# Optimization experiments

Hardware: AMD Instinct MI355X
Metric: run time of the kernel (lower is better)

The kernel has to match this reference:

```python
import jax, jax.numpy as jnp
import numpy as np

HEADS = 8
DIM_HEAD = 64
EPS = 1e-4
SCALE = DIM_HEAD ** -0.5


def setup_inputs() -> dict:
    key = jax.random.key(0)
    k1, k2, k3, k4 = jax.random.split(key, 4)
    dim = HEADS * DIM_HEAD  # 512
    x = jax.random.normal(k1, (2, 2048, dim), dtype=jnp.float32)
    # torch Linear weights are [out, in]; scale like default init
    Wq = jax.random.normal(k2, (dim, dim), dtype=jnp.float32) / np.sqrt(dim)
    Wkv = jax.random.normal(k3, (2 * dim, dim), dtype=jnp.float32) / np.sqrt(dim)
    Wout = jax.random.normal(k4, (dim, dim), dtype=jnp.float32) / np.sqrt(dim)
    return {"x": x, "Wq": Wq, "Wkv": Wkv, "Wout": Wout}


def _normalize_magnitude(t, eps=EPS):
    # divide by (sqrt(mean(t^2, -1)) + eps)
    mag = jnp.sqrt(jnp.mean(t * t, axis=-1, keepdims=True)) + eps
    return t / mag


def reference(x, Wq, Wkv, Wout):
    b, n, dim = x.shape
    h, d = HEADS, DIM_HEAD
    # norm=False -> Identity; context = x (self-attention)
    q = x @ Wq.T                      # [b, n, h*d]
    kv = x @ Wkv.T                    # [b, n, 2*h*d]
    k, v = jnp.split(kv, 2, axis=-1)
    def to_heads(t):
        return t.reshape(b, n, h, d).transpose(0, 2, 1, 3)  # [b, h, n, d]
    q, k, v = map(to_heads, (q, k, v))
    q = _normalize_magnitude(q)
    k = _normalize_magnitude(k)
    sim = jnp.einsum('bhid,bhjd->bhij', q, k) * SCALE
    attn = jax.nn.softmax(sim, axis=-1)
    out = jnp.einsum('bhij,bhjd->bhid', attn, v)
    out = out.transpose(0, 2, 1, 3).reshape(b, n, h * d)
    return out @ Wout.T
```

## Files before the change

### kernel.cpp

```cpp
#include <hip/hip_runtime.h>

typedef __bf16 bf16x8 __attribute__((ext_vector_type(8)));
typedef __bf16 bf16x4 __attribute__((ext_vector_type(4)));
typedef float  f32x4  __attribute__((ext_vector_type(4)));

#define LOG2E_F 1.44269504088896340736f

static constexpr int kB = 2, kN = 2048, kH = 8, kD = 64, kDim = 512;
static constexpr int kTok = kB * kN;
static constexpr int kNQKV = 1536;
static constexpr int kKH = 3;

__device__ __forceinline__ void gld16(const void* g, void* l) {
  __builtin_amdgcn_global_load_lds(
      (const __attribute__((address_space(1))) void*)g,
      (__attribute__((address_space(3))) void*)l, 16, 0, 0);
}


__global__ __launch_bounds__(256) void cvt_all(const float* __restrict__ x,
                                               const float* __restrict__ wq,
                                               const float* __restrict__ wkv,
                                               const float* __restrict__ wo,
                                               __bf16* __restrict__ xb,
                                               __bf16* __restrict__ wqkvb,
                                               __bf16* __restrict__ wob) {
  size_t i = ((size_t)blockIdx.x * 256 + threadIdx.x) * 8;
  const float* s; __bf16* d; size_t off;
  if (i < 2097152)      { s = x;   d = xb;              off = i; }
  else if (i < 2359296) { s = wq;  d = wqkvb;           off = i - 2097152; }
  else if (i < 2883584) { s = wkv; d = wqkvb + 262144;  off = i - 2359296; }
  else                  { s = wo;  d = wob;             off = i - 2883584; }
  float4 u = *(const float4*)(s + off);
  float4 v = *(const float4*)(s + off + 4);
  bf16x8 t;
  t[0] = (__bf16)u.x; t[1] = (__bf16)u.y; t[2] = (__bf16)u.z; t[3] = (__bf16)u.w;
  t[4] = (__bf16)v.x; t[5] = (__bf16)v.y; t[6] = (__bf16)v.z; t[7] = (__bf16)v.w;
  *(bf16x8*)(d + off) = t;
}

__global__ __launch_bounds__(256, 3) void gemm_qkv(const __bf16* __restrict__ A,
                                                   const __bf16* __restrict__ B,
                                                   __bf16* __restrict__ qn,
                                                   __bf16* __restrict__ kn,
                                                   __bf16* __restrict__ vt2) {
  const int K = kDim;
  const int tid = threadIdx.x;
  const int w = tid >> 6, lane = tid & 63, quad = lane >> 4, lq = lane & 15;
  const int m0 = blockIdx.y * 128;
  const int n0 = blockIdx.x * 64;
  const int wm = w * 32;
  __shared__ __bf16 As[2][128 * 64];
  __shared__ __bf16 Bs[2][64 * 64];

  const f32x4 zero = {0.f, 0.f, 0.f, 0.f};
  f32x4 acc[2][4];
#pragma unroll
  for (int fm = 0; fm < 2; ++fm)
#pragma unroll
    for (int fn = 0; fn < 4; ++fn) acc[fm][fn] = zero;

  const int sr = tid >> 3, ch = tid & 7;
  auto stage = [&](int k0, int buf) {
#pragma unroll
    for (int j = 0; j < 4; ++j) {
      const int row = j * 32 + sr;
      gld16(A + (size_t)(m0 + row) * K + k0 + ((ch ^ (row & 7)) << 3),
            &As[buf][row * 64 + ch * 8]);
    }
#pragma unroll
    for (int j = 0; j < 2; ++j) {
      const int row = j * 32 + sr;
      gld16(B + (size_t)(n0 + row) * K + k0 + ((ch ^ (row & 7)) << 3),
            &Bs[buf][row * 64 + ch * 8]);
    }
  };
  const int sw0 = ((quad ^ (lq & 7)) << 3);
  const int sw1 = (((4 | quad) ^ (lq & 7)) << 3);

  stage(0, 0);
  for (int i = 0; i < 8; ++i) {
    __syncthreads();
    if (i + 1 < 8) stage((i + 1) << 6, (i + 1) & 1);
    const __bf16* as = As[i & 1];
    const __bf16* bs = Bs[i & 1];
#pragma unroll
    for (int ks = 0; ks < 2; ++ks) {
      const int sw = ks ? sw1 : sw0;
      bf16x8 a[2], b[4];
#pragma unroll
      for (int fm = 0; fm < 2; ++fm)
        a[fm] = *(const bf16x8*)&as[(wm + fm * 16 + lq) * 64 + sw];
#pragma unroll
      for (int fn = 0; fn < 4; ++fn)
        b[fn] = *(const bf16x8*)&bs[(fn * 16 + lq) * 64 + sw];
#pragma unroll
      for (int fm = 0; fm < 2; ++fm)
#pragma unroll
        for (int fn = 0; fn < 4; ++fn)
          acc[fm][fn] =
              __builtin_amdgcn_mfma_f32_16x16x32_bf16(a[fm], b[fn], acc[fm][fn], 0, 0, 0);
    }
  }

  const int h = (n0 >> 6) & 7;
  if (n0 >= 1024) {
    __syncthreads();
    __bf16* Ts = &As[0][0];
#pragma unroll
    for (int fm = 0; fm < 2; ++fm)
#pragma unroll
      for (int r = 0; r < 4; ++r) {
        const int mo = wm + fm * 16 + quad * 4 + r;
        const int tau = mo >> 6, tt = mo & 63;
        const int p = (tt & 15) * 4 + (tt >> 4);
#pragma unroll
        for (int fn = 0; fn < 4; ++fn)
          Ts[tau * 4608 + (fn * 16 + lq) * 72 + p] = (__bf16)acc[fm][fn][r];
      }
    __syncthreads();
    const int b = m0 >> 11, kt0 = (m0 & (kN - 1)) >> 6;
    const int dd = tid >> 2, p0 = (tid & 3) << 4;
#pragma unroll
    for (int tau = 0; tau < 2; ++tau) {
      const __bf16* src = Ts + tau * 4608 + dd * 72 + p0;
      __bf16* dst = vt2 + ((size_t)((b * kH + h) * 32 + kt0 + tau)) * 4096 + tid * 16;
      *(bf16x8*)dst = *(const bf16x8*)src;
      *(bf16x8*)(dst + 8) = *(const bf16x8*)(src + 8);
    }
  } else {
    const float qs = (n0 < 512) ? (0.125f * LOG2E_F) : 1.0f;
    __bf16* dst0 = (n0 < 512) ? qn : kn;
#pragma unroll
    for (int fm = 0; fm < 2; ++fm)
#pragma unroll
      for (int r = 0; r < 4; ++r) {
        float ss = 0.f;
#pragma unroll
        for (int fn = 0; fn < 4; ++fn) ss += acc[fm][fn][r] * acc[fm][fn][r];
#pragma unroll
        for (int off = 1; off < 16; off <<= 1) ss += __shfl_xor(ss, off, 64);
        const float inv = qs / (sqrtf(ss * (1.f / 64)) + 1e-4f);
        const int m = m0 + wm + fm * 16 + quad * 4 + r;
        const int b = m >> 11, n = m & (kN - 1);
        __bf16* dst = dst0 + ((size_t)(b * kH + h) * kN + n) * kD;
#pragma unroll
        for (int fn = 0; fn < 4; ++fn)
          dst[fn * 16 + lq] = (__bf16)(acc[fm][fn][r] * inv);
      }
  }
}

__global__ __launch_bounds__(256, 3) void attn(const __bf16* __restrict__ qn,
                                               const __bf16* __restrict__ kn,
                                               const __bf16* __restrict__ vt2,
                                               __bf16* __restrict__ po,
                                               float* __restrict__ pl) {
  const int qt = blockIdx.x, bh = blockIdx.y, kh = blockIdx.z;
  const int kt0 = kh * 11;
  const int cnt = (kh == 2) ? 10 : 11;
  const int tid = threadIdx.x;
  const int w = tid >> 6, lane = tid & 63, quad = lane >> 4, lq = lane & 15;
  __shared__ __bf16 Ks[2][4096];
  __shared__ __bf16 Vs[2][4096];
  __shared__ __bf16 Ps[4][32 * 72];
  __bf16* myP = Ps[w];

  bf16x8 aq[2][2];
#pragma unroll
  for (int fm = 0; fm < 2; ++fm) {
    const __bf16* Qb = qn + ((size_t)bh * kN + qt * 128 + w * 32 + fm * 16 + lq) * kD;
    aq[fm][0] = *(const bf16x8*)(Qb + quad * 8);
    aq[fm][1] = *(const bf16x8*)(Qb + 32 + quad * 8);
  }

  const f32x4 zero  = {0.f, 0.f, 0.f, 0.f};
  const f32x4 minit = {-12.f, -12.f, -12.f, -12.f};
  f32x4 o[2][4];
  float lr[2][4];
#pragma unroll
  for (int fm = 0; fm < 2; ++fm)
#pragma unroll
    for (int i = 0; i < 4; ++i) { o[fm][i] = zero; lr[fm][i] = 0.f; }

  const __bf16* Kb = kn + (size_t)bh * kN * kD;
  const __bf16* Vb = vt2 + (size_t)bh * 32 * 4096;

  auto stage = [&](int ktg, int buf) {
#pragma unroll
    for (int j = 0; j < 2; ++j) {
      const int s = j * 256 + tid;
      const int row = s >> 3, ch = s & 7;
      const int src = row * 64 + ((ch ^ (row & 7)) << 3);
      gld16(Kb + (size_t)ktg * 4096 + src, &Ks[buf][s * 8]);
      gld16(Vb + (size_t)ktg * 4096 + src, &Vs[buf][s * 8]);
    }
  };
  const int sw0 = ((quad ^ (lq & 7)) << 3);
  const int sw1 = (((4 | quad) ^ (lq & 7)) << 3);

  stage(kt0, 0);
  for (int kt = 0; kt < cnt; ++kt) {
    __syncthreads();
    if (kt + 1 < cnt) stage(kt0 + kt + 1, (kt + 1) & 1);
    const __bf16* ks_ = Ks[kt & 1];
    const __bf16* vs_ = Vs[kt & 1];

    bf16x8 kb0[4], kb1[4], vb0[4], vb1[4];
#pragma unroll
    for (int fn = 0; fn < 4; ++fn) {
      const int rb = (fn * 16 + lq) * 64;
      kb0[fn] = *(const bf16x8*)&ks_[rb + sw0];
      kb1[fn] = *(const bf16x8*)&ks_[rb + sw1];
      vb0[fn] = *(const bf16x8*)&vs_[rb + sw0];
      vb1[fn] = *(const bf16x8*)&vs_[rb + sw1];
    }
    f32x4 s[2][4];
#pragma unroll
    for (int fm = 0; fm < 2; ++fm)
#pragma unroll
      for (int fn = 0; fn < 4; ++fn) {
        f32x4 a = __builtin_amdgcn_mfma_f32_16x16x32_bf16(aq[fm][0], kb0[fn], minit, 0, 0, 0);
        s[fm][fn] = __builtin_amdgcn_mfma_f32_16x16x32_bf16(aq[fm][1], kb1[fn], a, 0, 0, 0);
      }

#pragma unroll
    for (int fm = 0; fm < 2; ++fm)
#pragma unroll
      for (int r = 0; r < 4; ++r) {
        const float p0 = __builtin_amdgcn_exp2f(s[fm][0][r]);
        const float p1 = __builtin_amdgcn_exp2f(s[fm][1][r]);
        const float p2 = __builtin_amdgcn_exp2f(s[fm][2][r]);
        const float p3 = __builtin_amdgcn_exp2f(s[fm][3][r]);
        lr[fm][r] += (p0 + p1) + (p2 + p3);
        bf16x4 pk = {(__bf16)p0, (__bf16)p1, (__bf16)p2, (__bf16)p3};
        *(bf16x4*)&myP[(fm * 16 + quad * 4 + r) * 72 + lq * 4] = pk;
      }

#pragma unroll
    for (int fm = 0; fm < 2; ++fm) {
      bf16x8 ap0 = *(const bf16x8*)&myP[(fm * 16 + lq) * 72 + quad * 8];
      bf16x8 ap1 = *(const bf16x8*)&myP[(fm * 16 + lq) * 72 + 32 + quad * 8];
#pragma unroll
      for (int fn = 0; fn < 4; ++fn) {
        o[fm][fn] = __builtin_amdgcn_mfma_f32_16x16x32_bf16(ap0, vb0[fn], o[fm][fn], 0, 0, 0);
        o[fm][fn] = __builtin_amdgcn_mfma_f32_16x16x32_bf16(ap1, vb1[fn], o[fm][fn], 0, 0, 0);
      }
    }
  }

  const int b = bh >> 3, h = bh & 7;
#pragma unroll
  for (int fm = 0; fm < 2; ++fm) {
    const int qrow0 = qt * 128 + w * 32 + fm * 16 + quad * 4;
#pragma unroll
    for (int r = 0; r < 4; ++r) {
      float sum = lr[fm][r];
#pragma unroll
      for (int off = 1; off < 16; off <<= 1) sum += __shfl_xor(sum, off, 64);
      if (lq == 0) pl[(size_t)kh * 32768 + bh * kN + qrow0 + r] = sum;
      const size_t ob = ((size_t)kh * kTok + b * kN + qrow0 + r) * kDim + h * 64;
#pragma unroll
      for (int fn = 0; fn < 4; ++fn) po[ob + fn * 16 + lq] = (__bf16)o[fm][fn][r];
    }
  }
}

__global__ __launch_bounds__(256) void combine(const __bf16* __restrict__ po,
                                               const float* __restrict__ pl,
                                               __bf16* __restrict__ ao) {
  const size_t i = ((size_t)blockIdx.x * 256 + threadIdx.x) * 4;
  const int tok = (int)(i >> 9), dk = (int)(i & 511);
  const int h = dk >> 6, b = tok >> 11, qrow = tok & (kN - 1);
  const int idx = (b * kH + h) * kN + qrow;
  float l = 0.f;
#pragma unroll
  for (int kh = 0; kh < kKH; ++kh) l += pl[kh * 32768 + idx];
  const float inv = 1.f / l;
  float s0 = 0.f, s1 = 0.f, s2 = 0.f, s3 = 0.f;
#pragma unroll
  for (int kh = 0; kh < kKH; ++kh) {
    bf16x4 a = *(const bf16x4*)(po + (size_t)kh * kTok * kDim + i);
    s0 += (float)a[0]; s1 += (float)a[1]; s2 += (float)a[2]; s3 += (float)a[3];
  }
  bf16x4 t = {(__bf16)(s0 * inv), (__bf16)(s1 * inv),
              (__bf16)(s2 * inv), (__bf16)(s3 * inv)};
  *(bf16x4*)(ao + i) = t;
}

__global__ __launch_bounds__(256, 2) void gemm64(const __bf16* __restrict__ A,
                                                 const __bf16* __restrict__ B,
                                                 float* __restrict__ C,
                                                 int N, int K) {
  const int tid = threadIdx.x;
  const int w = tid >> 6, lane = tid & 63, quad = lane >> 4, lq = lane & 15;
  const int m0 = blockIdx.y * 64;
  const int n0 = blockIdx.x * 64;
  const int wm = (w >> 1) * 32, wn = (w & 1) * 32;
  __shared__ __bf16 As[2][4096];
  __shared__ __bf16 Bs[2][4096];

  const f32x4 zero = {0.f, 0.f, 0.f, 0.f};
  f32x4 acc00 = zero, acc01 = zero, acc10 = zero, acc11 = zero;

  const int sr = tid >> 3, ch = tid & 7;
  auto stage = [&](int k0, int buf) {
#pragma unroll
    for (int j = 0; j < 2; ++j) {
      const int row = j * 32 + sr;
      const int src = k0 + ((ch ^ (row & 7)) << 3);
      gld16(A + (size_t)(m0 + row) * K + src, &As[buf][row * 64 + ch * 8]);
      gld16(B + (size_t)(n0 + row) * K + src, &Bs[buf][row * 64 + ch * 8]);
    }
  };
  const int sw0 = ((quad ^ (lq & 7)) << 3);
  const int sw1 = (((4 | quad) ^ (lq & 7)) << 3);

  stage(0, 0);
  const int iters = K >> 6;
  for (int i = 0; i < iters; ++i) {
    __syncthreads();
    if (i + 1 < iters) stage((i + 1) << 6, (i + 1) & 1);
    const __bf16* as = As[i & 1];
    const __bf16* bs = Bs[i & 1];
#pragma unroll
    for (int ks = 0; ks < 2; ++ks) {
      const int sw = ks ? sw1 : sw0;
      bf16x8 a0 = *(const bf16x8*)&as[(wm +      lq) * 64 + sw];
      bf16x8 a1 = *(const bf16x8*)&as[(wm + 16 + lq) * 64 + sw];
      bf16x8 b0 = *(const bf16x8*)&bs[(wn +      lq) * 64 + sw];
      bf16x8 b1 = *(const bf16x8*)&bs[(wn + 16 + lq) * 64 + sw];
      acc00 = __builtin_amdgcn_mfma_f32_16x16x32_bf16(a0, b0, acc00, 0, 0, 0);
      acc01 = __builtin_amdgcn_mfma_f32_16x16x32_bf16(a0, b1, acc01, 0, 0, 0);
      acc10 = __builtin_amdgcn_mfma_f32_16x16x32_bf16(a1, b0, acc10, 0, 0, 0);
      acc11 = __builtin_amdgcn_mfma_f32_16x16x32_bf16(a1, b1, acc11, 0, 0, 0);
    }
  }
  const f32x4 av[2][2] = {{acc00, acc01}, {acc10, acc11}};
#pragma unroll
  for (int fm = 0; fm < 2; ++fm)
#pragma unroll
    for (int fn = 0; fn < 2; ++fn)
#pragma unroll
      for (int r = 0; r < 4; ++r)
        C[(size_t)(m0 + wm + fm * 16 + quad * 4 + r) * N + (n0 + wn + fn * 16 + lq)] =
            av[fm][fn][r];
}

extern "C" void kernel_launch(void* const* d_in, const int* in_sizes, int n_in,
                              void* d_out, int out_size, void* d_ws, size_t ws_size,
                              hipStream_t stream) {
  const float* x    = (const float*)d_in[0];
  const float* Wq   = (const float*)d_in[1];
  const float* Wkv  = (const float*)d_in[2];
  const float* Wout = (const float*)d_in[3];
  float* out = (float*)d_out;
  char* ws = (char*)d_ws;

  __bf16* xb    = (__bf16*)(ws);
  __bf16* wqkvb = (__bf16*)(ws + (size_t)(4 << 20));
  __bf16* wob   = (__bf16*)(ws + (size_t)(6 << 20));
  __bf16* qn    = (__bf16*)(ws + (size_t)(7 << 20));
  __bf16* kn    = (__bf16*)(ws + (size_t)(11 << 20));
  __bf16* vt2   = (__bf16*)(ws + (size_t)(15 << 20));
  __bf16* po    = (__bf16*)(ws + (size_t)(19 << 20));
  float*  pl    = (float*)(ws + (size_t)(32 << 20));
  __bf16* ao    = (__bf16*)(ws + (size_t)(33 << 20));

  cvt_all<<<1536, 256, 0, stream>>>(x, Wq, Wkv, Wout, xb, wqkvb, wob);
  gemm_qkv<<<dim3(kNQKV / 64, kTok / 128), 256, 0, stream>>>(xb, wqkvb, qn, kn, vt2);
  attn<<<dim3(kN / 128, kB * kH, kKH), 256, 0, stream>>>(qn, kn, vt2, po, pl);
  combine<<<kTok * kDim / 1024, 256, 0, stream>>>(po, pl, ao);
  gemm64<<<dim3(kDim / 64, kTok / 64), 256, 0, stream>>>(ao, wob, out, kDim, kDim);
}
```

Measured before the change: 118.3 us.

## Enlarge QKV GEMM and attention tiles, split keys four ways

The QKV projection GEMM now uses 128x128 tiles in one shared buffer, with each wave computing a 64x64 sub-tile, and its V-transpose epilogue handles two heads per block. The attention kernel now has each wave process 64 query rows instead of 32, and the key range is split into four equal chunks of 8 tiles instead of three uneven ones. V fragment loads are deferred until after the softmax. The intent is more MFMA work per shared-memory load and fewer blocks, at the cost of more registers (launch bounds lowered to 2), fewer blocks in flight, and a larger partial-output buffer for the combine step.

```diff
diff --git a/kernel.cpp b/kernel.cpp
--- a/kernel.cpp
+++ b/kernel.cpp
@@ -9,7 +9,7 @@
 static constexpr int kB = 2, kN = 2048, kH = 8, kD = 64, kDim = 512;
 static constexpr int kTok = kB * kN;
 static constexpr int kNQKV = 1536;
-static constexpr int kKH = 3;
+static constexpr int kKH = 4;
 
 __device__ __forceinline__ void gld16(const void* g, void* l) {
   __builtin_amdgcn_global_load_lds(
@@ -39,7 +39,7 @@
   *(bf16x8*)(d + off) = t;
 }
 
-__global__ __launch_bounds__(256, 3) void gemm_qkv(const __bf16* __restrict__ A,
+__global__ __launch_bounds__(256, 2) void gemm_qkv(const __bf16* __restrict__ A,
                                                    const __bf16* __restrict__ B,
                                                    __bf16* __restrict__ qn,
                                                    __bf16* __restrict__ kn,
@@ -48,31 +48,25 @@
   const int tid = threadIdx.x;
   const int w = tid >> 6, lane = tid & 63, quad = lane >> 4, lq = lane & 15;
   const int m0 = blockIdx.y * 128;
-  const int n0 = blockIdx.x * 64;
-  const int wm = w * 32;
-  __shared__ __bf16 As[2][128 * 64];
-  __shared__ __bf16 Bs[2][64 * 64];
+  const int n0 = blockIdx.x * 128;
+  const int wm = (w >> 1) * 64, wn = (w & 1) * 64;
+  __shared__ __bf16 shm[32768];
 
   const f32x4 zero = {0.f, 0.f, 0.f, 0.f};
-  f32x4 acc[2][4];
-#pragma unroll
-  for (int fm = 0; fm < 2; ++fm)
+  f32x4 acc[4][4];
+#pragma unroll
+  for (int fm = 0; fm < 4; ++fm)
 #pragma unroll
     for (int fn = 0; fn < 4; ++fn) acc[fm][fn] = zero;
 
-  const int sr = tid >> 3, ch = tid & 7;
   auto stage = [&](int k0, int buf) {
 #pragma unroll
     for (int j = 0; j < 4; ++j) {
-      const int row = j * 32 + sr;
-      gld16(A + (size_t)(m0 + row) * K + k0 + ((ch ^ (row & 7)) << 3),
-            &As[buf][row * 64 + ch * 8]);
-    }
-#pragma unroll
-    for (int j = 0; j < 2; ++j) {
-      const int row = j * 32 + sr;
-      gld16(B + (size_t)(n0 + row) * K + k0 + ((ch ^ (row & 7)) << 3),
-            &Bs[buf][row * 64 + ch * 8]);
+      const int s = j * 256 + tid;
+      const int row = s >> 3, ch = s & 7;
+      const int off = k0 + ((ch ^ (row & 7)) << 3);
+      gld16(A + (size_t)(m0 + row) * K + off, &shm[buf * 8192 + s * 8]);
+      gld16(B + (size_t)(n0 + row) * K + off, &shm[16384 + buf * 8192 + s * 8]);
     }
   };
   const int sw0 = ((quad ^ (lq & 7)) << 3);
@@ -81,21 +75,20 @@
   stage(0, 0);
   for (int i = 0; i < 8; ++i) {
     __syncthreads();
-    if (i + 1 < 8) stage((i + 1) << 6, (i + 1) & 1);
-    const __bf16* as = As[i & 1];
-    const __bf16* bs = Bs[i & 1];
+    if (i < 7) stage((i + 1) << 6, (i + 1) & 1);
+    const int ab = (i & 1) * 8192;
 #pragma unroll
     for (int ks = 0; ks < 2; ++ks) {
       const int sw = ks ? sw1 : sw0;
-      bf16x8 a[2], b[4];
-#pragma unroll
-      for (int fm = 0; fm < 2; ++fm)
-        a[fm] = *(const bf16x8*)&as[(wm + fm * 16 + lq) * 64 + sw];
+      bf16x8 a[4], b[4];
+#pragma unroll
+      for (int fm = 0; fm < 4; ++fm)
+        a[fm] = *(const bf16x8*)&shm[ab + (wm + fm * 16 + lq) * 64 + sw];
 #pragma unroll
       for (int fn = 0; fn < 4; ++fn)
-        b[fn] = *(const bf16x8*)&bs[(fn * 16 + lq) * 64 + sw];
-#pragma unroll
-      for (int fm = 0; fm < 2; ++fm)
+        b[fn] = *(const bf16x8*)&shm[16384 + ab + (wn + fn * 16 + lq) * 64 + sw];
+#pragma unroll
+      for (int fm = 0; fm < 4; ++fm)
 #pragma unroll
         for (int fn = 0; fn < 4; ++fn)
           acc[fm][fn] =
@@ -103,36 +96,39 @@
     }
   }
 
-  const int h = (n0 >> 6) & 7;
+  const int nb = n0 + wn;
   if (n0 >= 1024) {
     __syncthreads();
-    __bf16* Ts = &As[0][0];
-#pragma unroll
-    for (int fm = 0; fm < 2; ++fm)
+    const int hh = wn >> 6;
+    const int b = m0 >> 11, kt0 = (m0 & (kN - 1)) >> 6;
+#pragma unroll
+    for (int fm = 0; fm < 4; ++fm)
 #pragma unroll
       for (int r = 0; r < 4; ++r) {
         const int mo = wm + fm * 16 + quad * 4 + r;
-        const int tau = mo >> 6, tt = mo & 63;
+        const int rh = mo >> 6, tt = mo & 63;
         const int p = (tt & 15) * 4 + (tt >> 4);
 #pragma unroll
         for (int fn = 0; fn < 4; ++fn)
-          Ts[tau * 4608 + (fn * 16 + lq) * 72 + p] = (__bf16)acc[fm][fn][r];
-      }
-    __syncthreads();
-    const int b = m0 >> 11, kt0 = (m0 & (kN - 1)) >> 6;
+          shm[(hh * 2 + rh) * 4608 + (fn * 16 + lq) * 72 + p] = (__bf16)acc[fm][fn][r];
+      }
+    __syncthreads();
     const int dd = tid >> 2, p0 = (tid & 3) << 4;
-#pragma unroll
-    for (int tau = 0; tau < 2; ++tau) {
-      const __bf16* src = Ts + tau * 4608 + dd * 72 + p0;
-      __bf16* dst = vt2 + ((size_t)((b * kH + h) * 32 + kt0 + tau)) * 4096 + tid * 16;
+    const int hbase = (n0 >> 6) & 7;
+#pragma unroll
+    for (int t = 0; t < 4; ++t) {
+      const __bf16* src = &shm[t * 4608 + dd * 72 + p0];
+      __bf16* dst = vt2 +
+          ((size_t)((b * kH + hbase + (t >> 1)) * 32 + kt0 + (t & 1))) * 4096 + tid * 16;
       *(bf16x8*)dst = *(const bf16x8*)src;
       *(bf16x8*)(dst + 8) = *(const bf16x8*)(src + 8);
     }
   } else {
-    const float qs = (n0 < 512) ? (0.125f * LOG2E_F) : 1.0f;
-    __bf16* dst0 = (n0 < 512) ? qn : kn;
-#pragma unroll
-    for (int fm = 0; fm < 2; ++fm)
+    const int h = (nb >> 6) & 7;
+    const float qs = (nb < 512) ? (0.125f * LOG2E_F) : 1.0f;
+    __bf16* dst0 = (nb < 512) ? qn : kn;
+#pragma unroll
+    for (int fm = 0; fm < 4; ++fm)
 #pragma unroll
       for (int r = 0; r < 4; ++r) {
         float ss = 0.f;
@@ -151,35 +147,33 @@
   }
 }
 
-__global__ __launch_bounds__(256, 3) void attn(const __bf16* __restrict__ qn,
+__global__ __launch_bounds__(256, 2) void attn(const __bf16* __restrict__ qn,
                                                const __bf16* __restrict__ kn,
                                                const __bf16* __restrict__ vt2,
                                                __bf16* __restrict__ po,
                                                float* __restrict__ pl) {
   const int qt = blockIdx.x, bh = blockIdx.y, kh = blockIdx.z;
-  const int kt0 = kh * 11;
-  const int cnt = (kh == 2) ? 10 : 11;
   const int tid = threadIdx.x;
   const int w = tid >> 6, lane = tid & 63, quad = lane >> 4, lq = lane & 15;
   __shared__ __bf16 Ks[2][4096];
   __shared__ __bf16 Vs[2][4096];
-  __shared__ __bf16 Ps[4][32 * 72];
-  __bf16* myP = Ps[w];
-
-  bf16x8 aq[2][2];
-#pragma unroll
-  for (int fm = 0; fm < 2; ++fm) {
-    const __bf16* Qb = qn + ((size_t)bh * kN + qt * 128 + w * 32 + fm * 16 + lq) * kD;
+  __shared__ __bf16 Ps[4][64 * 72];
+  __bf16* myP = &Ps[w][0];
+
+  bf16x8 aq[4][2];
+#pragma unroll
+  for (int fm = 0; fm < 4; ++fm) {
+    const __bf16* Qb = qn + ((size_t)bh * kN + qt * 256 + w * 64 + fm * 16 + lq) * kD;
     aq[fm][0] = *(const bf16x8*)(Qb + quad * 8);
     aq[fm][1] = *(const bf16x8*)(Qb + 32 + quad * 8);
   }
 
   const f32x4 zero  = {0.f, 0.f, 0.f, 0.f};
   const f32x4 minit = {-12.f, -12.f, -12.f, -12.f};
-  f32x4 o[2][4];
-  float lr[2][4];
-#pragma unroll
-  for (int fm = 0; fm < 2; ++fm)
+  f32x4 o[4][4];
+  float lr[4][4];
+#pragma unroll
+  for (int fm = 0; fm < 4; ++fm)
 #pragma unroll
     for (int i = 0; i < 4; ++i) { o[fm][i] = zero; lr[fm][i] = 0.f; }
 
@@ -199,46 +193,49 @@
   const int sw0 = ((quad ^ (lq & 7)) << 3);
   const int sw1 = (((4 | quad) ^ (lq & 7)) << 3);
 
+  const int kt0 = kh * 8;
   stage(kt0, 0);
-  for (int kt = 0; kt < cnt; ++kt) {
-    __syncthreads();
-    if (kt + 1 < cnt) stage(kt0 + kt + 1, (kt + 1) & 1);
-    const __bf16* ks_ = Ks[kt & 1];
-    const __bf16* vs_ = Vs[kt & 1];
-
-    bf16x8 kb0[4], kb1[4], vb0[4], vb1[4];
+  for (int kt = 0; kt < 8; ++kt) {
+    __syncthreads();
+    if (kt < 7) stage(kt0 + kt + 1, (kt + 1) & 1);
+    const __bf16* ks_ = &Ks[kt & 1][0];
+    const __bf16* vs_ = &Vs[kt & 1][0];
+
+    bf16x8 kb0[4], kb1[4];
 #pragma unroll
     for (int fn = 0; fn < 4; ++fn) {
       const int rb = (fn * 16 + lq) * 64;
       kb0[fn] = *(const bf16x8*)&ks_[rb + sw0];
       kb1[fn] = *(const bf16x8*)&ks_[rb + sw1];
-      vb0[fn] = *(const bf16x8*)&vs_[rb + sw0];
-      vb1[fn] = *(const bf16x8*)&vs_[rb + sw1];
-    }
-    f32x4 s[2][4];
-#pragma unroll
-    for (int fm = 0; fm < 2; ++fm)
+    }
+#pragma unroll
+    for (int fm = 0; fm < 4; ++fm) {
+      f32x4 s[4];
 #pragma unroll
       for (int fn = 0; fn < 4; ++fn) {
         f32x4 a = __builtin_amdgcn_mfma_f32_16x16x32_bf16(aq[fm][0], kb0[fn], minit, 0, 0, 0);
-        s[fm][fn] = __builtin_amdgcn_mfma_f32_16x16x32_bf16(aq[fm][1], kb1[fn], a, 0, 0, 0);
-      }
-
-#pragma unroll
-    for (int fm = 0; fm < 2; ++fm)
+        s[fn] = __builtin_amdgcn_mfma_f32_16x16x32_bf16(aq[fm][1], kb1[fn], a, 0, 0, 0);
+      }
 #pragma unroll
       for (int r = 0; r < 4; ++r) {
-        const float p0 = __builtin_amdgcn_exp2f(s[fm][0][r]);
-        const float p1 = __builtin_amdgcn_exp2f(s[fm][1][r]);
-        const float p2 = __builtin_amdgcn_exp2f(s[fm][2][r]);
-        const float p3 = __builtin_amdgcn_exp2f(s[fm][3][r]);
+        const float p0 = __builtin_amdgcn_exp2f(s[0][r]);
+        const float p1 = __builtin_amdgcn_exp2f(s[1][r]);
+        const float p2 = __builtin_amdgcn_exp2f(s[2][r]);
+        const float p3 = __builtin_amdgcn_exp2f(s[3][r]);
         lr[fm][r] += (p0 + p1) + (p2 + p3);
         bf16x4 pk = {(__bf16)p0, (__bf16)p1, (__bf16)p2, (__bf16)p3};
         *(bf16x4*)&myP[(fm * 16 + quad * 4 + r) * 72 + lq * 4] = pk;
       }
-
-#pragma unroll
-    for (int fm = 0; fm < 2; ++fm) {
+    }
+    bf16x8 vb0[4], vb1[4];
+#pragma unroll
+    for (int fn = 0; fn < 4; ++fn) {
+      const int rb = (fn * 16 + lq) * 64;
+      vb0[fn] = *(const bf16x8*)&vs_[rb + sw0];
+      vb1[fn] = *(const bf16x8*)&vs_[rb + sw1];
+    }
+#pragma unroll
+    for (int fm = 0; fm < 4; ++fm) {
       bf16x8 ap0 = *(const bf16x8*)&myP[(fm * 16 + lq) * 72 + quad * 8];
       bf16x8 ap1 = *(const bf16x8*)&myP[(fm * 16 + lq) * 72 + 32 + quad * 8];
 #pragma unroll
@@ -251,8 +248,8 @@
 
   const int b = bh >> 3, h = bh & 7;
 #pragma unroll
-  for (int fm = 0; fm < 2; ++fm) {
-    const int qrow0 = qt * 128 + w * 32 + fm * 16 + quad * 4;
+  for (int fm = 0; fm < 4; ++fm) {
+    const int qrow0 = qt * 256 + w * 64 + fm * 16 + quad * 4;
 #pragma unroll
     for (int r = 0; r < 4; ++r) {
       float sum = lr[fm][r];
@@ -321,8 +318,8 @@
   for (int i = 0; i < iters; ++i) {
     __syncthreads();
     if (i + 1 < iters) stage((i + 1) << 6, (i + 1) & 1);
-    const __bf16* as = As[i & 1];
-    const __bf16* bs = Bs[i & 1];
+    const __bf16* as = &As[i & 1][0];
+    const __bf16* bs = &Bs[i & 1][0];
 #pragma unroll
     for (int ks = 0; ks < 2; ++ks) {
       const int sw = ks ? sw1 : sw0;
@@ -364,12 +361,12 @@
   __bf16* kn    = (__bf16*)(ws + (size_t)(11 << 20));
   __bf16* vt2   = (__bf16*)(ws + (size_t)(15 << 20));
   __bf16* po    = (__bf16*)(ws + (size_t)(19 << 20));
-  float*  pl    = (float*)(ws + (size_t)(32 << 20));
-  __bf16* ao    = (__bf16*)(ws + (size_t)(33 << 20));
+  float*  pl    = (float*)(ws + (size_t)(35 << 20));
+  __bf16* ao    = (__bf16*)(ws + (size_t)(36 << 20));
 
   cvt_all<<<1536, 256, 0, stream>>>(x, Wq, Wkv, Wout, xb, wqkvb, wob);
-  gemm_qkv<<<dim3(kNQKV / 64, kTok / 128), 256, 0, stream>>>(xb, wqkvb, qn, kn, vt2);
-  attn<<<dim3(kN / 128, kB * kH, kKH), 256, 0, stream>>>(qn, kn, vt2, po, pl);
+  gemm_qkv<<<dim3(kNQKV / 128, kTok / 128), 256, 0, stream>>>(xb, wqkvb, qn, kn, vt2);
+  attn<<<dim3(kN / 256, kB * kH, kKH), 256, 0, stream>>>(qn, kn, vt2, po, pl);
   combine<<<kTok * kDim / 1024, 256, 0, stream>>>(po, pl, ao);
   gemm64<<<dim3(kDim / 64, kTok / 64), 256, 0, stream>>>(ao, wob, out, kDim, kDim);
 }
```

Measured after the change: 118.9 us. About the same (+0.5%).
